# Kernel optimization log

Measured on AMD Instinct MI355X. Metric: run time of the kernel, lower is better.

## Reference

```python
import jax, jax.numpy as jnp
import numpy as np

B, F, M, D = 64, 4, 4096, 1024
ITERS = 15

def _sign(x):
    # bipolar quantize: sign with sign(0) = +1
    return jnp.where(x >= 0, 1.0, -1.0).astype(x.dtype)

def setup_inputs() -> dict:
    key = jax.random.key(0)
    k1, k2, k3 = jax.random.split(key, 3)
    # bipolar (+1/-1) hypervectors, MAP/software VSA
    input = _sign(jax.random.normal(k1, (B, D), dtype=jnp.float32))
    init_estimates = _sign(jax.random.normal(k2, (B, F, D), dtype=jnp.float32))
    codebooks = _sign(jax.random.normal(k3, (F, M, D), dtype=jnp.float32))
    return {"input": input, "init_estimates": init_estimates, "codebooks": codebooks}

def reference(input, init_estimates, codebooks):
    # Concurrent resonator network (bipolar MAP VSA):
    #  bind = elementwise multiply, inverse = identity, multibind = product over factors.
    #  inv_others[b,f,:] = prod_{j != f} estimates[b,j,:] == (prod_all) * estimates  (since e*e = 1)
    def step(carry, _):
        est, converged, iters = carry
        total = jnp.prod(est, axis=-2, keepdims=True)          # (b,1,d)
        inv_others = total * est                                # (b,f,d) product of the other factors
        new_est = input[:, None, :] * inv_others                # unbind: (b,f,d)
        sim = jnp.einsum('bfd,fmd->bfm', new_est, codebooks)    # dot similarity vs each codebook
        upd = _sign(jnp.einsum('bfm,fmd->bfd', sim, codebooks)) # multiset weighted bundle + quantize
        now_conv = jnp.all(upd == est)                          # estimates stopped changing
        est2 = jnp.where(converged, est, upd)                   # freeze after convergence
        iters2 = iters + jnp.where(converged, 0, 1)
        return (est2, converged | now_conv, iters2), None

    init = (init_estimates, jnp.array(False), jnp.array(0, jnp.int32))
    (est, conv, iters), _ = jax.lax.scan(step, init, None, length=ITERS)
    # cleanup: argmax(|similarity|) per factor -> codebook indices
    sim = jnp.einsum('bfd,fmd->bfm', est, codebooks)
    outcome = jnp.argmax(jnp.abs(sim), axis=-1)                 # (b,f) int
    return outcome, est, iters, conv
```

## Files before the change

### kernel.cpp

```cpp
#include <hip/hip_runtime.h>
#include <hip/hip_fp16.h>

#define B_ 64
#define F_ 4
#define M_ 4096
#define D_ 1024
#define W_ 16
#define CW_ 64
#define NITER 15
#define NBLK 64
#define FPAD 16

typedef _Float16 f16;
typedef _Float16 f16x8 __attribute__((ext_vector_type(8)));
typedef float f32x4 __attribute__((ext_vector_type(4)));
typedef unsigned int u32;
typedef unsigned short u16;
typedef unsigned long long u64;

#define LD_AG(p)     __hip_atomic_load((p), __ATOMIC_RELAXED, __HIP_MEMORY_SCOPE_AGENT)
#define ST_AG(p, v)  __hip_atomic_store((p), (v), __ATOMIC_RELAXED, __HIP_MEMORY_SCOPE_AGENT)

__device__ __align__(16) u64 g_cbBits[F_ * M_ * W_];
__device__ __align__(16) u64 g_colBits[F_ * D_ * CW_];
__device__ __align__(16) f16 g_G[F_ * D_ * D_];
__device__ __align__(16) u64 g_inBits[B_ * W_];
__device__ __align__(16) u64 g_est[2][B_ * F_ * W_];
__device__ int g_done[NITER][NBLK * FPAD];
__device__ int g_mism[NITER][NBLK * FPAD];

__device__ __forceinline__ u32 nib16(u32 x) {
    x &= 0x0F0F0F0Fu;
    x = (x | (x >> 4)) & 0x00FF00FFu;
    x = (x | (x >> 8)) & 0x0000FFFFu;
    return x;
}

__global__ __launch_bounds__(256) void k_pack(const float* __restrict__ inp,
                                              const float* __restrict__ est0,
                                              const float* __restrict__ cb) {
    __shared__ unsigned char nib[4096];
    int blk = blockIdx.x, tid = threadIdx.x;
    int wv = tid >> 6, lane = tid & 63;
    const float* src; u64* dst; int r0;
    if (blk < 1024)      { src = cb;   dst = g_cbBits; r0 = blk * 16; }
    else if (blk < 1040) { src = est0; dst = g_est[0]; r0 = (blk - 1024) * 16; }
    else if (blk < 1044) { src = inp;  dst = g_inBits; r0 = (blk - 1040) * 16; }
    else {
        int idx = (blk - 1044) * 256 + tid;
        const int n = NITER * NBLK * FPAD;
        if (idx < n) ((int*)g_done)[idx] = 0;
        else if (idx < 2 * n) ((int*)g_mism)[idx - n] = 0;
        return;
    }
    int rw = r0 + wv * 4;
    unsigned char* mynib = nib + wv * 1024;
    #pragma unroll
    for (int rr = 0; rr < 4; rr++) {
        const float4* s4 = (const float4*)(src + (size_t)(rw + rr) * D_);
        #pragma unroll
        for (int it = 0; it < 4; it++) {
            float4 v = s4[it * 64 + lane];
            u32 n = (__float_as_uint(v.x) >> 31)
                  | (((__float_as_uint(v.y) >> 31)) << 1)
                  | (((__float_as_uint(v.z) >> 31)) << 2)
                  | (((__float_as_uint(v.w) >> 31)) << 3);
            mynib[rr * 256 + it * 64 + lane] = (unsigned char)n;
        }
    }
    uint4 q = *(const uint4*)(mynib + (lane >> 4) * 256 + (lane & 15) * 16);
    u32 w0 = nib16(q.x), w1 = nib16(q.y), w2 = nib16(q.z), w3 = nib16(q.w);
    u64 word = (u64)(w0 | (w1 << 16)) | ((u64)(w2 | (w3 << 16)) << 32);
    dst[(size_t)(rw + (lane >> 4)) * W_ + (lane & 15)] = word;
}

__global__ __launch_bounds__(256) void k_bitT() {
    int tid = threadIdx.x, wv = tid >> 6, lane = tid & 63;
    int tbase = (blockIdx.x * 4 + wv) * 4;
    for (int q = 0; q < 4; q++) {
        int task = tbase + q;
        int mt = task & 63;
        int wd = (task >> 6) & 15;
        int f  = task >> 10;
        u64 row = g_cbBits[((size_t)(f * M_ + mt * 64 + lane)) * W_ + wd];
        u64 myout = 0;
        #pragma unroll
        for (int j = 0; j < 64; j++) {
            u64 t = __ballot((row >> j) & 1ULL);
            if (lane == j) myout = t;
        }
        g_colBits[((size_t)(f * D_ + wd * 64 + lane)) * CW_ + mt] = myout;
    }
}

__global__ __launch_bounds__(256) void k_G() {
    int blk = blockIdx.x;
    int f = blk / 136;
    int pi = blk % 136;
    int t1 = 0;
    while (pi >= 16 - t1) { pi -= 16 - t1; t1++; }
    int t2 = t1 + pi;
    __shared__ u64 L1T[64][64];
    __shared__ u64 L2T[64][64];
    int tid = threadIdx.x;
    int wv = tid >> 6, lane = tid & 63;
    for (int it = 0; it < 16; it++) {
        int w = it * 4 + wv;
        L1T[w][lane] = g_colBits[((size_t)(f * D_ + t1 * 64 + lane)) * CW_ + w];
        L2T[w][lane] = g_colBits[((size_t)(f * D_ + t2 * 64 + lane)) * CW_ + w];
    }
    __syncthreads();
    int g1 = tid >> 4, g2 = tid & 15;
    int p[4][4] = {};
    for (int w = 0; w < 64; w++) {
        u64 a0 = L1T[w][g1], a1 = L1T[w][g1 + 16], a2 = L1T[w][g1 + 32], a3 = L1T[w][g1 + 48];
        u64 b0 = L2T[w][g2], b1 = L2T[w][g2 + 16], b2 = L2T[w][g2 + 32], b3 = L2T[w][g2 + 48];
        p[0][0] += __popcll(a0 ^ b0); p[0][1] += __popcll(a0 ^ b1);
        p[0][2] += __popcll(a0 ^ b2); p[0][3] += __popcll(a0 ^ b3);
        p[1][0] += __popcll(a1 ^ b0); p[1][1] += __popcll(a1 ^ b1);
        p[1][2] += __popcll(a1 ^ b2); p[1][3] += __popcll(a1 ^ b3);
        p[2][0] += __popcll(a2 ^ b0); p[2][1] += __popcll(a2 ^ b1);
        p[2][2] += __popcll(a2 ^ b2); p[2][3] += __popcll(a2 ^ b3);
        p[3][0] += __popcll(a3 ^ b0); p[3][1] += __popcll(a3 ^ b1);
        p[3][2] += __popcll(a3 ^ b2); p[3][3] += __popcll(a3 ^ b3);
    }
    #pragma unroll
    for (int i = 0; i < 4; i++) {
        int d1 = t1 * 64 + g1 + 16 * i;
        #pragma unroll
        for (int j = 0; j < 4; j++) {
            int d2 = t2 * 64 + g2 + 16 * j;
            g_G[((size_t)(f * D_ + d1)) * D_ + d2] = (f16)(M_ - 2 * p[i][j]);
        }
    }
    if (t1 == t2) return;
    __syncthreads();
    f16* Lt = (f16*)L1T;
    #pragma unroll
    for (int i = 0; i < 4; i++)
        #pragma unroll
        for (int j = 0; j < 4; j++)
            Lt[(g2 + 16 * j) * 72 + (g1 + 16 * i)] = (f16)(M_ - 2 * p[i][j]);
    __syncthreads();
    int r = tid >> 2, c0 = (tid & 3) * 16;
    const uint4* s = (const uint4*)&Lt[r * 72 + c0];
    uint4 v0 = s[0], v1 = s[1];
    uint4* dsto = (uint4*)&g_G[((size_t)(f * D_ + t2 * 64 + r)) * D_ + t1 * 64 + c0];
    dsto[0] = v0; dsto[1] = v1;
}

__device__ __forceinline__ u32 pairval(u32 bits, int i) {
    return 0x3C003C00u | (((bits >> i) & 1u) << 15) | (((bits >> (i + 1)) & 1u) << 31);
}

__global__ __launch_bounds__(256) void k_loop(float* __restrict__ out) {
    int blk = blockIdx.x;
    int f = blk & 3, dg = blk >> 2;
    int tid = threadIdx.x;
    int wv = tid >> 6, lane = tid & 63;
    __shared__ u64 neL[64][17];
    __shared__ __align__(16) char ldsB[64 * 2048];
    __shared__ int red[256];
    {
        const char* gsrc = (const char*)(g_G + ((size_t)(f * D_ + dg * 64)) * D_);
        for (int i = tid; i < 8192; i += 256) {
            int row = i >> 7, col = i & 127;
            uint4 v = *(const uint4*)(gsrc + (size_t)row * 2048 + col * 16);
            *(uint4*)(ldsB + row * 2048 + ((col * 16) ^ ((row & 7) << 4))) = v;
        }
    }
    const unsigned char* neB = (const unsigned char*)neL;
    int dd = lane & 15, gg = lane >> 4;
    int aBase = (wv * 16 + dd) * 136 + gg;
    int p0 = tid, p1 = 256 + tid, p2 = 512 + tid, p3 = 768 + tid;
    u64 prev[4];
    if (dd == 0) {
        #pragma unroll
        for (int j = 0; j < 4; j++) {
            int b = wv * 16 + gg * 4 + j;
            prev[j] = g_est[0][(size_t)(b * 4 + f) * W_ + dg];
        }
    }
    int iters = 0, conv = 0;
    for (int t = 0; t < NITER; t++) {
        const u64* rb = g_est[t & 1];
        u64* wb = g_est[(t + 1) & 1];
        if (blk == 0) {
            if (t > 0 && tid < NBLK) {
                const int* mp = &g_mism[t - 1][tid * FPAD];
                int v = LD_AG(&mp[0]) | LD_AG(&mp[1]) | LD_AG(&mp[2]) | LD_AG(&mp[3]);
                u64 any = __ballot(v != 0);
                if (tid == 0 && any == 0) conv = 1;
            }
            if (tid == 0 && !conv) iters++;
        }
        {
            const char* rbB = (const char*)rb;
            const char* a0 = rbB + (size_t)(p0 >> 4) * 512 + (p0 & 15) * 8;
            const char* a1 = rbB + (size_t)(p1 >> 4) * 512 + (p1 & 15) * 8;
            const char* a2 = rbB + (size_t)(p2 >> 4) * 512 + (p2 & 15) * 8;
            const char* a3 = rbB + (size_t)(p3 >> 4) * 512 + (p3 & 15) * 8;
            u64 e00, e01, e02, e03, e10, e11, e12, e13;
            u64 e20, e21, e22, e23, e30, e31, e32, e33;
            asm volatile(
                "global_load_dwordx2 %0, %16, off sc0 sc1\n\t"
                "global_load_dwordx2 %1, %16, off offset:128 sc0 sc1\n\t"
                "global_load_dwordx2 %2, %16, off offset:256 sc0 sc1\n\t"
                "global_load_dwordx2 %3, %16, off offset:384 sc0 sc1\n\t"
                "global_load_dwordx2 %4, %17, off sc0 sc1\n\t"
                "global_load_dwordx2 %5, %17, off offset:128 sc0 sc1\n\t"
                "global_load_dwordx2 %6, %17, off offset:256 sc0 sc1\n\t"
                "global_load_dwordx2 %7, %17, off offset:384 sc0 sc1\n\t"
                "global_load_dwordx2 %8, %18, off sc0 sc1\n\t"
                "global_load_dwordx2 %9, %18, off offset:128 sc0 sc1\n\t"
                "global_load_dwordx2 %10, %18, off offset:256 sc0 sc1\n\t"
                "global_load_dwordx2 %11, %18, off offset:384 sc0 sc1\n\t"
                "global_load_dwordx2 %12, %19, off sc0 sc1\n\t"
                "global_load_dwordx2 %13, %19, off offset:128 sc0 sc1\n\t"
                "global_load_dwordx2 %14, %19, off offset:256 sc0 sc1\n\t"
                "global_load_dwordx2 %15, %19, off offset:384 sc0 sc1\n\t"
                "s_waitcnt vmcnt(0)"
                : "=&v"(e00), "=&v"(e01), "=&v"(e02), "=&v"(e03),
                  "=&v"(e10), "=&v"(e11), "=&v"(e12), "=&v"(e13),
                  "=&v"(e20), "=&v"(e21), "=&v"(e22), "=&v"(e23),
                  "=&v"(e30), "=&v"(e31), "=&v"(e32), "=&v"(e33)
                : "v"(a0), "v"(a1), "v"(a2), "v"(a3)
                : "memory");
            u64 x0 = g_inBits[(p0 >> 4) * W_ + (p0 & 15)] ^ e00 ^ e01 ^ e02 ^ e03;
            u64 x1 = g_inBits[(p1 >> 4) * W_ + (p1 & 15)] ^ e10 ^ e11 ^ e12 ^ e13;
            u64 x2 = g_inBits[(p2 >> 4) * W_ + (p2 & 15)] ^ e20 ^ e21 ^ e22 ^ e23;
            u64 x3 = g_inBits[(p3 >> 4) * W_ + (p3 & 15)] ^ e30 ^ e31 ^ e32 ^ e33;
            u64 f0 = (f == 0) ? e00 : (f == 1) ? e01 : (f == 2) ? e02 : e03;
            u64 f1 = (f == 0) ? e10 : (f == 1) ? e11 : (f == 2) ? e12 : e13;
            u64 f2 = (f == 0) ? e20 : (f == 1) ? e21 : (f == 2) ? e22 : e23;
            u64 f3 = (f == 0) ? e30 : (f == 1) ? e31 : (f == 2) ? e32 : e33;
            neL[p0 >> 4][p0 & 15] = x0 ^ f0;
            neL[p1 >> 4][p1 & 15] = x1 ^ f1;
            neL[p2 >> 4][p2 & 15] = x2 ^ f2;
            neL[p3 >> 4][p3 & 15] = x3 ^ f3;
        }
        __syncthreads();
        f32x4 acc[4][2] = {};
        #pragma unroll
        for (int c = 0; c < 32; c++) {
            u32 bits = neB[aBase + c * 4];
            f16x8 a;
            ((u32*)&a)[0] = pairval(bits, 0);
            ((u32*)&a)[1] = pairval(bits, 2);
            ((u32*)&a)[2] = pairval(bits, 4);
            ((u32*)&a)[3] = pairval(bits, 6);
            #pragma unroll
            for (int ct = 0; ct < 4; ct++) {
                int rowB = ct * 16 + dd;
                f16x8 bf = *(const f16x8*)(ldsB + rowB * 2048 +
                                           ((c * 64 + gg * 16) ^ ((rowB & 7) << 4)));
                acc[ct][c & 1] =
                    __builtin_amdgcn_mfma_f32_16x16x32_f16(a, bf, acc[ct][c & 1], 0, 0, 0);
            }
        }
        u64 msk[4][4];
        #pragma unroll
        for (int ct = 0; ct < 4; ct++)
            #pragma unroll
            for (int j = 0; j < 4; j++) {
                float v = acc[ct][0][j] + acc[ct][1][j];
                msk[ct][j] = __ballot(v < 0.0f);
            }
        int mm = 0;
        if (dd == 0) {
            #pragma unroll
            for (int j = 0; j < 4; j++) {
                int b = wv * 16 + gg * 4 + j;
                u64 nv = ((msk[0][j] >> (gg * 16)) & 0xFFFFu)
                       | (((msk[1][j] >> (gg * 16)) & 0xFFFFu) << 16)
                       | (((msk[2][j] >> (gg * 16)) & 0xFFFFu) << 32)
                       | (((msk[3][j] >> (gg * 16)) & 0xFFFFu) << 48);
                if (prev[j] != nv) mm = 1;
                prev[j] = nv;
                ST_AG(&wb[(size_t)(b * 4 + f) * W_ + dg], nv);
            }
        }
        u64 anym = __ballot(mm != 0);
        if (lane == 0 && anym)
            ST_AG(&g_mism[t][blk * FPAD + wv], 1);
        __syncthreads();
        if (tid == 0)
            ST_AG(&g_done[t][blk * FPAD], 1);
        if (tid < NBLK) {
            while (LD_AG(&g_done[t][tid * FPAD]) == 0) {}
        }
        __syncthreads();
    }
    const u64* eb_g = g_est[NITER & 1];
    if (blk == 0) {
        if (tid < NBLK) {
            const int* mp = &g_mism[NITER - 1][tid * FPAD];
            int v = LD_AG(&mp[0]) | LD_AG(&mp[1]) | LD_AG(&mp[2]) | LD_AG(&mp[3]);
            u64 any = __ballot(v != 0);
            if (tid == 0) {
                if (any == 0) conv = 1;
                out[256 + 262144] = (float)iters;
                out[256 + 262144 + 1] = (float)conv;
            }
        }
    }
    for (int s = 0; s < 4; s++) {
        int task = blk * 4 + s;
        int bb = task >> 2, ff = task & 3;
        for (int j = 0; j < 4; j++) {
            int d = j * 256 + tid;
            u64 w = LD_AG(&eb_g[(size_t)(bb * 4 + ff) * W_ + (d >> 6)]);
            out[256 + ((size_t)(bb * 4 + ff)) * D_ + d] = ((w >> (d & 63)) & 1) ? -1.0f : 1.0f;
        }
        u64 eb[W_];
        #pragma unroll
        for (int w = 0; w < W_; w++) eb[w] = LD_AG(&eb_g[(size_t)(bb * 4 + ff) * W_ + w]);
        int bestKey = -1;
        for (int j = 0; j < 16; j++) {
            int m = j * 256 + tid;
            int p = 0;
            #pragma unroll
            for (int w = 0; w < W_; w++)
                p += __popcll(eb[w] ^ g_cbBits[((size_t)(ff * M_ + m)) * W_ + w]);
            int sv = D_ - 2 * p;
            int a = sv < 0 ? -sv : sv;
            int key = (a << 12) | (4095 - m);
            if (key > bestKey) bestKey = key;
        }
        red[tid] = bestKey;
        __syncthreads();
        for (int off = 128; off > 0; off >>= 1) {
            if (tid < off) red[tid] = max(red[tid], red[tid + off]);
            __syncthreads();
        }
        if (tid == 0) out[bb * 4 + ff] = (float)(4095 - (red[0] & 0xFFF));
        __syncthreads();
    }
}

extern "C" void kernel_launch(void* const* d_in, const int* in_sizes, int n_in,
                              void* d_out, int out_size, void* d_ws, size_t ws_size,
                              hipStream_t stream) {
    (void)d_ws; (void)ws_size;
    const float* inp  = (const float*)d_in[0];
    const float* est0 = (const float*)d_in[1];
    const float* cb   = (const float*)d_in[2];
    float* out = (float*)d_out;

    int flagInts = 2 * NITER * NBLK * FPAD;
    int zeroBlks = (flagInts + 255) / 256;
    k_pack<<<1044 + zeroBlks, 256, 0, stream>>>(inp, est0, cb);
    k_bitT<<<256, 256, 0, stream>>>();
    k_G<<<544, 256, 0, stream>>>();
    k_loop<<<NBLK, 256, 0, stream>>>(out);
}
```

Baseline: 299.7 us.

## Transpose estimate bit layout, cache input bits in LDS, move convergence bookkeeping out of loop

```diff
diff --git a/kernel.cpp b/kernel.cpp
--- a/kernel.cpp
+++ b/kernel.cpp
@@ -9,7 +9,7 @@
 #define CW_ 64
 #define NITER 15
 #define NBLK 64
-#define FPAD 16
+#define FPAD 32
 
 typedef _Float16 f16;
 typedef _Float16 f16x8 __attribute__((ext_vector_type(8)));
@@ -25,7 +25,7 @@
 __device__ __align__(16) u64 g_colBits[F_ * D_ * CW_];
 __device__ __align__(16) f16 g_G[F_ * D_ * D_];
 __device__ __align__(16) u64 g_inBits[B_ * W_];
-__device__ __align__(16) u64 g_est[2][B_ * F_ * W_];
+__device__ __align__(16) u64 g_est[2][W_ * F_ * B_];
 __device__ int g_done[NITER][NBLK * FPAD];
 __device__ int g_mism[NITER][NBLK * FPAD];
 
@@ -42,9 +42,9 @@
     __shared__ unsigned char nib[4096];
     int blk = blockIdx.x, tid = threadIdx.x;
     int wv = tid >> 6, lane = tid & 63;
-    const float* src; u64* dst; int r0;
+    const float* src; u64* dst; int r0; int estmode = 0;
     if (blk < 1024)      { src = cb;   dst = g_cbBits; r0 = blk * 16; }
-    else if (blk < 1040) { src = est0; dst = g_est[0]; r0 = (blk - 1024) * 16; }
+    else if (blk < 1040) { src = est0; dst = g_est[0]; r0 = (blk - 1024) * 16; estmode = 1; }
     else if (blk < 1044) { src = inp;  dst = g_inBits; r0 = (blk - 1040) * 16; }
     else {
         int idx = (blk - 1044) * 256 + tid;
@@ -71,7 +71,10 @@
     uint4 q = *(const uint4*)(mynib + (lane >> 4) * 256 + (lane & 15) * 16);
     u32 w0 = nib16(q.x), w1 = nib16(q.y), w2 = nib16(q.z), w3 = nib16(q.w);
     u64 word = (u64)(w0 | (w1 << 16)) | ((u64)(w2 | (w3 << 16)) << 32);
-    dst[(size_t)(rw + (lane >> 4)) * W_ + (lane & 15)] = word;
+    int r = rw + (lane >> 4), w = lane & 15;
+    size_t oi = estmode ? (size_t)((w * 4 + (r & 3)) * 64 + (r >> 2))
+                        : (size_t)r * W_ + w;
+    dst[oi] = word;
 }
 
 __global__ __launch_bounds__(256) void k_bitT() {
@@ -159,6 +162,7 @@
     int tid = threadIdx.x;
     int wv = tid >> 6, lane = tid & 63;
     __shared__ u64 neL[64][17];
+    __shared__ u64 inL[64][17];
     __shared__ __align__(16) char ldsB[64 * 2048];
     __shared__ int red[256];
     {
@@ -168,76 +172,63 @@
             uint4 v = *(const uint4*)(gsrc + (size_t)row * 2048 + col * 16);
             *(uint4*)(ldsB + row * 2048 + ((col * 16) ^ ((row & 7) << 4))) = v;
         }
+        for (int i = tid; i < 1024; i += 256)
+            inL[i >> 4][i & 15] = g_inBits[i];
     }
     const unsigned char* neB = (const unsigned char*)neL;
     int dd = lane & 15, gg = lane >> 4;
     int aBase = (wv * 16 + dd) * 136 + gg;
-    int p0 = tid, p1 = 256 + tid, p2 = 512 + tid, p3 = 768 + tid;
+    int nb = tid & 63, wq = tid >> 6;
     u64 prev[4];
     if (dd == 0) {
         #pragma unroll
-        for (int j = 0; j < 4; j++) {
-            int b = wv * 16 + gg * 4 + j;
-            prev[j] = g_est[0][(size_t)(b * 4 + f) * W_ + dg];
-        }
-    }
-    int iters = 0, conv = 0;
+        for (int j = 0; j < 4; j++)
+            prev[j] = g_est[0][(dg * 4 + f) * 64 + (wv * 16 + gg * 4 + j)];
+    }
     for (int t = 0; t < NITER; t++) {
         const u64* rb = g_est[t & 1];
         u64* wb = g_est[(t + 1) & 1];
-        if (blk == 0) {
-            if (t > 0 && tid < NBLK) {
-                const int* mp = &g_mism[t - 1][tid * FPAD];
-                int v = LD_AG(&mp[0]) | LD_AG(&mp[1]) | LD_AG(&mp[2]) | LD_AG(&mp[3]);
-                u64 any = __ballot(v != 0);
-                if (tid == 0 && any == 0) conv = 1;
-            }
-            if (tid == 0 && !conv) iters++;
-        }
         {
-            const char* rbB = (const char*)rb;
-            const char* a0 = rbB + (size_t)(p0 >> 4) * 512 + (p0 & 15) * 8;
-            const char* a1 = rbB + (size_t)(p1 >> 4) * 512 + (p1 & 15) * 8;
-            const char* a2 = rbB + (size_t)(p2 >> 4) * 512 + (p2 & 15) * 8;
-            const char* a3 = rbB + (size_t)(p3 >> 4) * 512 + (p3 & 15) * 8;
+            const char* base0 = (const char*)rb + (size_t)wq * 8192 + (size_t)nb * 8;
+            const char* base1 = base0 + 4096;
             u64 e00, e01, e02, e03, e10, e11, e12, e13;
             u64 e20, e21, e22, e23, e30, e31, e32, e33;
             asm volatile(
                 "global_load_dwordx2 %0, %16, off sc0 sc1\n\t"
-                "global_load_dwordx2 %1, %16, off offset:128 sc0 sc1\n\t"
-                "global_load_dwordx2 %2, %16, off offset:256 sc0 sc1\n\t"
-                "global_load_dwordx2 %3, %16, off offset:384 sc0 sc1\n\t"
-                "global_load_dwordx2 %4, %17, off sc0 sc1\n\t"
-                "global_load_dwordx2 %5, %17, off offset:128 sc0 sc1\n\t"
-                "global_load_dwordx2 %6, %17, off offset:256 sc0 sc1\n\t"
-                "global_load_dwordx2 %7, %17, off offset:384 sc0 sc1\n\t"
-                "global_load_dwordx2 %8, %18, off sc0 sc1\n\t"
-                "global_load_dwordx2 %9, %18, off offset:128 sc0 sc1\n\t"
-                "global_load_dwordx2 %10, %18, off offset:256 sc0 sc1\n\t"
-                "global_load_dwordx2 %11, %18, off offset:384 sc0 sc1\n\t"
-                "global_load_dwordx2 %12, %19, off sc0 sc1\n\t"
-                "global_load_dwordx2 %13, %19, off offset:128 sc0 sc1\n\t"
-                "global_load_dwordx2 %14, %19, off offset:256 sc0 sc1\n\t"
-                "global_load_dwordx2 %15, %19, off offset:384 sc0 sc1\n\t"
+                "global_load_dwordx2 %1, %16, off offset:512 sc0 sc1\n\t"
+                "global_load_dwordx2 %2, %16, off offset:1024 sc0 sc1\n\t"
+                "global_load_dwordx2 %3, %16, off offset:1536 sc0 sc1\n\t"
+                "global_load_dwordx2 %4, %16, off offset:2048 sc0 sc1\n\t"
+                "global_load_dwordx2 %5, %16, off offset:2560 sc0 sc1\n\t"
+                "global_load_dwordx2 %6, %16, off offset:3072 sc0 sc1\n\t"
+                "global_load_dwordx2 %7, %16, off offset:3584 sc0 sc1\n\t"
+                "global_load_dwordx2 %8, %17, off sc0 sc1\n\t"
+                "global_load_dwordx2 %9, %17, off offset:512 sc0 sc1\n\t"
+                "global_load_dwordx2 %10, %17, off offset:1024 sc0 sc1\n\t"
+                "global_load_dwordx2 %11, %17, off offset:1536 sc0 sc1\n\t"
+                "global_load_dwordx2 %12, %17, off offset:2048 sc0 sc1\n\t"
+                "global_load_dwordx2 %13, %17, off offset:2560 sc0 sc1\n\t"
+                "global_load_dwordx2 %14, %17, off offset:3072 sc0 sc1\n\t"
+                "global_load_dwordx2 %15, %17, off offset:3584 sc0 sc1\n\t"
                 "s_waitcnt vmcnt(0)"
                 : "=&v"(e00), "=&v"(e01), "=&v"(e02), "=&v"(e03),
                   "=&v"(e10), "=&v"(e11), "=&v"(e12), "=&v"(e13),
                   "=&v"(e20), "=&v"(e21), "=&v"(e22), "=&v"(e23),
                   "=&v"(e30), "=&v"(e31), "=&v"(e32), "=&v"(e33)
-                : "v"(a0), "v"(a1), "v"(a2), "v"(a3)
+                : "v"(base0), "v"(base1)
                 : "memory");
-            u64 x0 = g_inBits[(p0 >> 4) * W_ + (p0 & 15)] ^ e00 ^ e01 ^ e02 ^ e03;
-            u64 x1 = g_inBits[(p1 >> 4) * W_ + (p1 & 15)] ^ e10 ^ e11 ^ e12 ^ e13;
-            u64 x2 = g_inBits[(p2 >> 4) * W_ + (p2 & 15)] ^ e20 ^ e21 ^ e22 ^ e23;
-            u64 x3 = g_inBits[(p3 >> 4) * W_ + (p3 & 15)] ^ e30 ^ e31 ^ e32 ^ e33;
+            u64 x0 = inL[nb][wq * 4 + 0] ^ e00 ^ e01 ^ e02 ^ e03;
+            u64 x1 = inL[nb][wq * 4 + 1] ^ e10 ^ e11 ^ e12 ^ e13;
+            u64 x2 = inL[nb][wq * 4 + 2] ^ e20 ^ e21 ^ e22 ^ e23;
+            u64 x3 = inL[nb][wq * 4 + 3] ^ e30 ^ e31 ^ e32 ^ e33;
             u64 f0 = (f == 0) ? e00 : (f == 1) ? e01 : (f == 2) ? e02 : e03;
             u64 f1 = (f == 0) ? e10 : (f == 1) ? e11 : (f == 2) ? e12 : e13;
             u64 f2 = (f == 0) ? e20 : (f == 1) ? e21 : (f == 2) ? e22 : e23;
             u64 f3 = (f == 0) ? e30 : (f == 1) ? e31 : (f == 2) ? e32 : e33;
-            neL[p0 >> 4][p0 & 15] = x0 ^ f0;
-            neL[p1 >> 4][p1 & 15] = x1 ^ f1;
-            neL[p2 >> 4][p2 & 15] = x2 ^ f2;
-            neL[p3 >> 4][p3 & 15] = x3 ^ f3;
+            neL[nb][wq * 4 + 0] = x0 ^ f0;
+            neL[nb][wq * 4 + 1] = x1 ^ f1;
+            neL[nb][wq * 4 + 2] = x2 ^ f2;
+            neL[nb][wq * 4 + 3] = x3 ^ f3;
         }
         __syncthreads();
         f32x4 acc[4][2] = {};
@@ -277,7 +268,7 @@
                        | (((msk[3][j] >> (gg * 16)) & 0xFFFFu) << 48);
                 if (prev[j] != nv) mm = 1;
                 prev[j] = nv;
-                ST_AG(&wb[(size_t)(b * 4 + f) * W_ + dg], nv);
+                ST_AG(&wb[(dg * 4 + f) * 64 + b], nv);
             }
         }
         u64 anym = __ballot(mm != 0);
@@ -292,16 +283,23 @@
         __syncthreads();
     }
     const u64* eb_g = g_est[NITER & 1];
-    if (blk == 0) {
-        if (tid < NBLK) {
-            const int* mp = &g_mism[NITER - 1][tid * FPAD];
+    if (blk == 0 && tid < NBLK) {
+        int anyt[NITER];
+        #pragma unroll
+        for (int t = 0; t < NITER; t++) {
+            const int* mp = &g_mism[t][tid * FPAD];
             int v = LD_AG(&mp[0]) | LD_AG(&mp[1]) | LD_AG(&mp[2]) | LD_AG(&mp[3]);
-            u64 any = __ballot(v != 0);
-            if (tid == 0) {
-                if (any == 0) conv = 1;
-                out[256 + 262144] = (float)iters;
-                out[256 + 262144 + 1] = (float)conv;
+            anyt[t] = (__ballot(v != 0) != 0);
+        }
+        if (tid == 0) {
+            int iters = 0, conv = 0;
+            #pragma unroll
+            for (int t = 0; t < NITER; t++) {
+                if (!conv) iters++;
+                if (!anyt[t]) conv = 1;
             }
+            out[256 + 262144] = (float)iters;
+            out[256 + 262144 + 1] = (float)conv;
         }
     }
     for (int s = 0; s < 4; s++) {
@@ -309,12 +307,12 @@
         int bb = task >> 2, ff = task & 3;
         for (int j = 0; j < 4; j++) {
             int d = j * 256 + tid;
-            u64 w = LD_AG(&eb_g[(size_t)(bb * 4 + ff) * W_ + (d >> 6)]);
+            u64 w = LD_AG(&eb_g[((d >> 6) * 4 + ff) * 64 + bb]);
             out[256 + ((size_t)(bb * 4 + ff)) * D_ + d] = ((w >> (d & 63)) & 1) ? -1.0f : 1.0f;
         }
         u64 eb[W_];
         #pragma unroll
-        for (int w = 0; w < W_; w++) eb[w] = LD_AG(&eb_g[(size_t)(bb * 4 + ff) * W_ + w]);
+        for (int w = 0; w < W_; w++) eb[w] = LD_AG(&eb_g[(w * 4 + ff) * 64 + bb]);
         int bestKey = -1;
         for (int j = 0; j < 16; j++) {
             int m = j * 256 + tid;
```

After: 303.4 us. No clear change (+1.2%).
